# Optimization experiments

Measured on AMD Instinct MI355X. Metric: run time of the kernel, lower is better.

The kernel has to match this reference:

```python
import jax, jax.numpy as jnp
import numpy as np

B, T, CIN, C = 64, 1, 2048, 2048


def setup_inputs() -> dict:
    key = jax.random.key(0)
    ks = jax.random.split(key, 6)
    x = jax.random.normal(ks[0], (B, T, CIN), jnp.float32)
    Wq = jax.random.normal(ks[1], (C, CIN), jnp.float32) * 0.02
    bq = jax.random.normal(ks[2], (C,), jnp.float32) * 0.02
    Wk = jax.random.normal(ks[3], (C, CIN), jnp.float32) * 0.02
    bk = jax.random.normal(ks[4], (C,), jnp.float32) * 0.02
    Wv = jax.random.normal(ks[5], (C, CIN), jnp.float32) * 0.02
    return {"x": x, "Wq": Wq, "bq": bq, "Wk": Wk, "bk": bk, "Wv": Wv, "pos": 3}


def _rope(t, cos, sin, rot, swap):
    # q_y = (-q1, q0, -q3, q2, ...): multiply by (+1,-1,...) then swap pairs
    t_y = jnp.take(t * rot, swap, axis=-1)
    return t * cos + t_y * sin


def reference(x, Wq, bq, Wk, bk, Wv, pos):
    Cout = Wq.shape[0]
    # thetas = 10000^(-2*i) for i in [0, Cout//2), as in the source
    idx = jnp.arange(Cout // 2, dtype=jnp.float32)
    thetas = 10000.0 ** (-2.0 * idx)
    p = jnp.float32(pos)
    cos = jnp.repeat(jnp.cos(p * thetas), 2)  # repeat_interleave(2) -> [Cout]
    sin = jnp.repeat(jnp.sin(p * thetas), 2)
    i = jnp.arange(Cout)
    rot = jnp.where(i % 2 == 0, 1.0, -1.0).astype(x.dtype)
    swap = jnp.where(i % 2 == 0, i + 1, i - 1)

    q = x @ Wq.T + bq            # [B,T,C]
    k = x @ Wk.T + bk            # [B,T,C]
    v = x @ Wv.T                 # [B,T,C] (no bias)

    q = _rope(q, cos, sin, rot, swap)
    k = _rope(k, cos, sin, rot, swap)

    dk = 1.0 / jnp.sqrt(jnp.float32(Cout))
    q = jax.nn.elu(q * dk) + 1.0
    k = jax.nn.elu(k * dk) + 1.0

    memory = jnp.einsum('btc,btd->bcd', k, v)         # k^T v state update, [B,C,C]
    zeta = jnp.swapaxes(k, -2, -1)                    # k^T, [B,C,T]
    scale = jnp.einsum('btc,bcs->bts', q, zeta)       # [B,T,T] (T=1)
    mem_read = jnp.einsum('btc,bcd->btd', q, memory)  # [B,T,C]
    return mem_read / scale
```

## Files before the change

kernel.cpp:

```cpp
#include <hip/hip_runtime.h>


#define ND 2048
#define KD 2048
#define K4 (KD / 4)

__global__ __launch_bounds__(256)
void vgemm(const float* __restrict__ x, const float* __restrict__ Wv,
           float* __restrict__ out) {
    const int lane = threadIdx.x & 63;
    const int wid  = threadIdx.x >> 6;
    const int bid  = blockIdx.x;
    const int nO   = (bid & 7) + ((bid >> 4) << 3);
    const int half = (bid >> 3) & 1;
    const int n0   = nO * 8;
    const int b0   = (half * 4 + wid) * 8;

    const float4* __restrict__ xq = (const float4*)x;
    const float4* __restrict__ wq = (const float4*)Wv;

    float acc[64];
#pragma unroll
    for (int j = 0; j < 64; ++j) acc[j] = 0.0f;

#pragma unroll
    for (int i = 0; i < 8; ++i) {
        const int k4 = (i << 6) + lane;
        float4 xr[8], wr[8];
#pragma unroll
        for (int bb = 0; bb < 8; ++bb)
            xr[bb] = xq[(size_t)(b0 + bb) * K4 + k4];
#pragma unroll
        for (int nn = 0; nn < 8; ++nn)
            wr[nn] = wq[(size_t)(n0 + nn) * K4 + k4];
#pragma unroll
        for (int bb = 0; bb < 8; ++bb)
#pragma unroll
            for (int nn = 0; nn < 8; ++nn) {
                float a = acc[bb * 8 + nn];
                a = fmaf(xr[bb].x, wr[nn].x, a);
                a = fmaf(xr[bb].y, wr[nn].y, a);
                a = fmaf(xr[bb].z, wr[nn].z, a);
                a = fmaf(xr[bb].w, wr[nn].w, a);
                acc[bb * 8 + nn] = a;
            }
    }

    __shared__ float red[4][64][64];
    float* myrow = &red[wid][lane][0];
    const int swz = lane & 31;
#pragma unroll
    for (int j = 0; j < 64; ++j) myrow[j ^ swz] = acc[j];
    __syncthreads();

    float s = 0.0f;
#pragma unroll
    for (int l = 0; l < 64; ++l) s += red[wid][l][lane ^ (l & 31)];

    out[(size_t)(b0 + (lane >> 3)) * ND + n0 + (lane & 7)] = s;
}

extern "C" void kernel_launch(void* const* d_in, const int* in_sizes, int n_in,
                              void* d_out, int out_size, void* d_ws, size_t ws_size,
                              hipStream_t stream) {
    const float* x  = (const float*)d_in[0];
    const float* Wv = (const float*)d_in[5];
    float* out = (float*)d_out;

    vgemm<<<512, 256, 0, stream>>>(x, Wv, out);
}
```

Baseline: 100.8 us.

## Split K across blocks, reduce with wave shuffles, remap blocks per XCD

Splits the K dimension of the x·Wv^T GEMM in two across twice as many blocks, writing partial results to the workspace and summing them in a separate combine kernel. Replaces the shared-memory transpose reduction with a butterfly __shfl_xor reduction inside each wavefront. Remaps block IDs so each XCD handles a contiguous range of output columns, and adds an occupancy hint to the launch bounds. The split-K path adds a second launch and a round trip of partial sums through global memory. It falls back to a single-pass kernel when no workspace is provided.

```diff
diff --git a/kernel.cpp b/kernel.cpp
--- a/kernel.cpp
+++ b/kernel.cpp
@@ -5,17 +5,11 @@
 #define KD 2048
 #define K4 (KD / 4)
 
-__global__ __launch_bounds__(256)
-void vgemm(const float* __restrict__ x, const float* __restrict__ Wv,
-           float* __restrict__ out) {
-    const int lane = threadIdx.x & 63;
-    const int wid  = threadIdx.x >> 6;
-    const int bid  = blockIdx.x;
-    const int nO   = (bid & 7) + ((bid >> 4) << 3);
-    const int half = (bid >> 3) & 1;
-    const int n0   = nO * 8;
-    const int b0   = (half * 4 + wid) * 8;
-
+template <int NI>
+__device__ __forceinline__ void gemm_body(const float* __restrict__ x,
+                                          const float* __restrict__ Wv,
+                                          float* __restrict__ dst,
+                                          int n0, int b0, int kbase, int lane) {
     const float4* __restrict__ xq = (const float4*)x;
     const float4* __restrict__ wq = (const float4*)Wv;
 
@@ -24,8 +18,8 @@
     for (int j = 0; j < 64; ++j) acc[j] = 0.0f;
 
 #pragma unroll
-    for (int i = 0; i < 8; ++i) {
-        const int k4 = (i << 6) + lane;
+    for (int i = 0; i < NI; ++i) {
+        const int k4 = kbase + (i << 6) + lane;
         float4 xr[8], wr[8];
 #pragma unroll
         for (int bb = 0; bb < 8; ++bb)
@@ -46,18 +40,57 @@
             }
     }
 
-    __shared__ float red[4][64][64];
-    float* myrow = &red[wid][lane][0];
-    const int swz = lane & 31;
 #pragma unroll
-    for (int j = 0; j < 64; ++j) myrow[j ^ swz] = acc[j];
-    __syncthreads();
+    for (int s = 0; s < 6; ++s) {
+        const int bit = (lane >> s) & 1;
+#pragma unroll
+        for (int u = 0; u < (64 >> (s + 1)); ++u) {
+            float snd = bit ? acc[2 * u] : acc[2 * u + 1];
+            float kep = bit ? acc[2 * u + 1] : acc[2 * u];
+            acc[u] = kep + __shfl_xor(snd, 1 << s, 64);
+        }
+    }
 
-    float s = 0.0f;
-#pragma unroll
-    for (int l = 0; l < 64; ++l) s += red[wid][l][lane ^ (l & 31)];
+    dst[(size_t)(b0 + (lane >> 3)) * ND + n0 + (lane & 7)] = acc[0];
+}
 
-    out[(size_t)(b0 + (lane >> 3)) * ND + n0 + (lane & 7)] = s;
+__global__ __launch_bounds__(256, 3)
+void vgemm_ks(const float* __restrict__ x, const float* __restrict__ Wv,
+              float* __restrict__ part) {
+    const int lane = threadIdx.x & 63;
+    const int wid  = threadIdx.x >> 6;
+    const int bid  = blockIdx.x;
+    const int xcd  = bid & 7;
+    const int r    = bid >> 3;
+    const int nO   = xcd * 32 + (r & 31);
+    const int bh   = (r >> 5) & 1;
+    const int kh   = r >> 6;
+    gemm_body<4>(x, Wv, part + (size_t)kh * (64 * ND),
+                 nO * 8, (bh * 4 + wid) * 8, kh * 256, lane);
+}
+
+__global__ __launch_bounds__(256, 3)
+void vgemm_full(const float* __restrict__ x, const float* __restrict__ Wv,
+                float* __restrict__ out) {
+    const int lane = threadIdx.x & 63;
+    const int wid  = threadIdx.x >> 6;
+    const int bid  = blockIdx.x;
+    const int xcd  = bid & 7;
+    const int r    = bid >> 3;
+    const int nO   = xcd * 32 + (r & 31);
+    const int bh   = r >> 5;
+    gemm_body<8>(x, Wv, out, nO * 8, (bh * 4 + wid) * 8, 0, lane);
+}
+
+__global__ __launch_bounds__(256)
+void combine(const float* __restrict__ part, float* __restrict__ out) {
+    const int t = blockIdx.x * 256 + threadIdx.x;
+    const float4* __restrict__ p = (const float4*)part;
+    float4 a = p[t];
+    float4 b = p[t + 32768];
+    float4 o;
+    o.x = a.x + b.x; o.y = a.y + b.y; o.z = a.z + b.z; o.w = a.w + b.w;
+    ((float4*)out)[t] = o;
 }
 
 extern "C" void kernel_launch(void* const* d_in, const int* in_sizes, int n_in,
@@ -67,5 +100,12 @@
     const float* Wv = (const float*)d_in[5];
     float* out = (float*)d_out;
 
-    vgemm<<<512, 256, 0, stream>>>(x, Wv, out);
+    const size_t partBytes = 2ull * 64 * ND * sizeof(float);
+    if (d_ws && ws_size >= partBytes) {
+        float* part = (float*)d_ws;
+        vgemm_ks<<<1024, 256, 0, stream>>>(x, Wv, part);
+        combine<<<128, 256, 0, stream>>>(part, out);
+    } else {
+        vgemm_full<<<512, 256, 0, stream>>>(x, Wv, out);
+    }
 }
```

Result: slower. 121.0 us (+20.0%).
